# Optimization experiments

Measured on AMD Instinct MI355X. Metric: run time of the kernel, lower is better.

Reference implementation:

```python
import jax, jax.numpy as jnp
import numpy as np

N = 50000
E = 800000
IN_C, C1, C2 = 256, 128, 64
BN_EPS = 1e-5


def setup_inputs() -> dict:
    key = jax.random.key(0)
    ks = jax.random.split(key, 12)
    x = jax.random.normal(ks[0], (N, IN_C), dtype=jnp.float32)
    edge_index = jax.random.randint(ks[1], (2, E), 0, N, dtype=jnp.int32)
    edge_weight = jax.random.uniform(ks[2], (E,), dtype=jnp.float32)
    W1 = jax.random.normal(ks[3], (IN_C, C1), dtype=jnp.float32) * 0.05
    b1 = jnp.zeros((C1,), dtype=jnp.float32)
    W2 = jax.random.normal(ks[4], (C1, C2), dtype=jnp.float32) * 0.05
    b2 = jnp.zeros((C2,), dtype=jnp.float32)
    g1 = jnp.ones((C1,), dtype=jnp.float32)
    be1 = jnp.zeros((C1,), dtype=jnp.float32)
    g2 = jnp.ones((C2,), dtype=jnp.float32)
    be2 = jnp.zeros((C2,), dtype=jnp.float32)
    Ws = jax.random.normal(ks[5], (IN_C, C2), dtype=jnp.float32) * 0.05
    bs = jnp.zeros((C2,), dtype=jnp.float32)
    return dict(x=x, edge_index=edge_index, edge_weight=edge_weight,
                W1=W1, b1=b1, W2=W2, b2=b2, g1=g1, be1=be1, g2=g2, be2=be2,
                Ws=Ws, bs=bs)


def _gcn_conv(h_in, row, col, ew, W, b):
    # PyG GCNConv: transform then symmetric-normalized aggregation with self-loops
    n = h_in.shape[0]
    h = h_in @ W  # [N, C]
    loop = jnp.arange(n, dtype=row.dtype)
    row_f = jnp.concatenate([row, loop])
    col_f = jnp.concatenate([col, loop])
    ew_f = jnp.concatenate([ew, jnp.ones((n,), dtype=ew.dtype)])
    deg = jax.ops.segment_sum(ew_f, col_f, num_segments=n)  # degree at targets
    dinv = jnp.where(deg > 0, jax.lax.rsqrt(deg), 0.0)
    norm = dinv[row_f] * ew_f * dinv[col_f]  # [E+N]
    out = jax.ops.segment_sum(h[row_f] * norm[:, None], col_f, num_segments=n)
    return out + b


def _batchnorm(x, gamma, beta):
    mu = jnp.mean(x, axis=0)
    var = jnp.mean(jnp.square(x - mu), axis=0)  # biased, as torch BN forward
    return (x - mu) * jax.lax.rsqrt(var + BN_EPS) * gamma + beta


def reference(x, edge_index, edge_weight, W1, b1, W2, b2, g1, be1, g2, be2, Ws, bs):
    row, col = edge_index[0], edge_index[1]
    skip = x @ Ws + bs
    x1 = _gcn_conv(x, row, col, edge_weight, W1, b1)
    x1 = jax.nn.gelu(_batchnorm(x1, g1, be1), approximate=False)
    # dropout is identity in deterministic/eval reference
    x2 = _gcn_conv(x1, row, col, edge_weight, W2, b2)
    x2 = _batchnorm(x2, g2, be2) + skip
    return x2
```

## Files before the change

kernel.cpp:

```cpp
#include <hip/hip_runtime.h>
#include <math.h>

constexpr int NN = 50000;
constexpr int EE = 800000;
constexpr int INC = 256, CC1 = 128, CC2 = 64;

typedef short bf16x8 __attribute__((ext_vector_type(8)));
typedef float f32x4 __attribute__((ext_vector_type(4)));

__device__ __forceinline__ unsigned short f2bf(float f) {
    unsigned int u = __builtin_bit_cast(unsigned int, f);
    u = (u + 0x7FFFu + ((u >> 16) & 1u)) >> 16;
    return (unsigned short)u;
}
__device__ __forceinline__ float bflo(unsigned int w) {
    return __builtin_bit_cast(float, w << 16);
}
__device__ __forceinline__ float bfhi(unsigned int w) {
    return __builtin_bit_cast(float, w & 0xFFFF0000u);
}


__global__ void init_kernel(unsigned long long* __restrict__ packed,
                            float* __restrict__ stats, int* __restrict__ cursor, int n) {
    int i = blockIdx.x * 256 + threadIdx.x;
    if (i < 1024) stats[i] = 0.0f;
    if (i == 0) *cursor = 0;
    if (i < n) packed[i] = 0ULL;
}

__global__ void rank_kernel(const int* __restrict__ col, const float* __restrict__ ew,
                            unsigned long long* __restrict__ packed, int* __restrict__ rank,
                            int e_cnt) {
    int e = blockIdx.x * 256 + threadIdx.x;
    if (e < e_cnt) {
        int c = col[e];
        unsigned int fx = __float2uint_rn(ew[e] * 16777216.0f);
        unsigned long long old = atomicAdd(&packed[c], (1ULL << 32) | (unsigned long long)fx);
        rank[e] = (int)(old >> 32);
    }
}

__global__ void alloc_kernel(const unsigned long long* __restrict__ packed,
                             float* __restrict__ dinv, int* __restrict__ start,
                             int* __restrict__ count, int* __restrict__ cursor, int n) {
    int i = blockIdx.x * 256 + threadIdx.x;
    if (i < n) {
        unsigned long long p = packed[i];
        int cnt = (int)(p >> 32);
        float deg = 1.0f + (float)(unsigned int)(p & 0xFFFFFFFFu) * (1.0f / 16777216.0f);
        dinv[i] = rsqrtf(deg);
        count[i] = cnt;
        start[i] = atomicAdd(cursor, cnt);
    }
}

__global__ void fill_kernel(const int* __restrict__ row, const int* __restrict__ col,
                            const float* __restrict__ ew, const float* __restrict__ dinv,
                            const int* __restrict__ rank, const int* __restrict__ start,
                            int2* __restrict__ pairs, int e_cnt) {
    int e = blockIdx.x * 256 + threadIdx.x;
    if (e < e_cnt) {
        int r = row[e], c = col[e];
        float nv = dinv[r] * ew[e] * dinv[c];
        int pos = start[c] + rank[e];
        pairs[pos] = make_int2(r, __float_as_int(nv));
    }
}

template<int K, int N1, int N2, int AMODE>
__global__ void __launch_bounds__(256) mfma_gemm(const void* __restrict__ Av,
        const float* __restrict__ B1, const float* __restrict__ B2,
        unsigned short* __restrict__ C1, float* __restrict__ C2,
        const float* __restrict__ scA, const float* __restrict__ shA, int n_rows) {
    constexpr int NT = N1 + N2;
    constexpr int NG = 64;
    constexpr int KC = K / 8;
    constexpr int PITCH = K + 8;
    __shared__ unsigned short Blds[NG * PITCH];

    const int tid = threadIdx.x;
    const int wave = tid >> 6, lane = tid & 63;
    const int quad = lane >> 4, nIdx = lane & 15;
    const int row0 = blockIdx.x * 64 + wave * 16;
    const int arow = row0 + nIdx;
    const int arow_c = (arow < n_rows) ? arow : (n_rows - 1);

    bf16x8 afrag[K / 32];
    if (AMODE == 1) {
        const unsigned short* A = (const unsigned short*)Av;
        const unsigned short* ap = A + (long long)arow_c * K + quad * 8;
#pragma unroll
        for (int s = 0; s < K / 32; s++)
            afrag[s] = *(const bf16x8*)(ap + s * 32);
    } else {
        const float* A = (const float*)Av;
        const float* ap = A + (long long)arow_c * K + quad * 8;
#pragma unroll
        for (int s = 0; s < K / 32; s++) {
            float4 lo = *(const float4*)(ap + s * 32);
            float4 hi = *(const float4*)(ap + s * 32 + 4);
            float v[8] = {lo.x, lo.y, lo.z, lo.w, hi.x, hi.y, hi.z, hi.w};
            if (AMODE == 2) {
                int kb = s * 32 + quad * 8;
                float4 s0 = *(const float4*)(scA + kb);
                float4 s1 = *(const float4*)(scA + kb + 4);
                float4 t0 = *(const float4*)(shA + kb);
                float4 t1 = *(const float4*)(shA + kb + 4);
                float sc[8] = {s0.x, s0.y, s0.z, s0.w, s1.x, s1.y, s1.z, s1.w};
                float sh[8] = {t0.x, t0.y, t0.z, t0.w, t1.x, t1.y, t1.z, t1.w};
#pragma unroll
                for (int j = 0; j < 8; j++) {
                    float u = v[j] * sc[j] + sh[j];
                    v[j] = u * 0.5f * (1.0f + erff(u * 0.70710678f));
                }
            }
            bf16x8 f;
#pragma unroll
            for (int j = 0; j < 8; j++) f[j] = (short)f2bf(v[j]);
            afrag[s] = f;
        }
    }

    for (int g0 = 0; g0 < NT; g0 += NG) {
        if (g0) __syncthreads();
        {
            int n = tid & 63;
            int col = g0 + n;
            const float* Bp = B1; int Nw = N1; int bcol = col;
            if (N2 > 0 && col >= N1) { Bp = B2; Nw = N2; bcol = col - N1; }
            for (int kc = tid >> 6; kc < KC; kc += 4) {
                int k0 = kc * 8;
                bf16x8 v;
#pragma unroll
                for (int j = 0; j < 8; j++)
                    v[j] = (short)f2bf(Bp[(long long)(k0 + j) * Nw + bcol]);
                *(bf16x8*)(&Blds[n * PITCH + k0]) = v;
            }
        }
        __syncthreads();
#pragma unroll
        for (int t = 0; t < NG / 16; t++) {
            const unsigned short* bp = &Blds[(t * 16 + nIdx) * PITCH + quad * 8];
            f32x4 acc = {0.0f, 0.0f, 0.0f, 0.0f};
#pragma unroll
            for (int s = 0; s < K / 32; s++) {
                bf16x8 bf = *(const bf16x8*)(bp + s * 32);
                acc = __builtin_amdgcn_mfma_f32_16x16x32_bf16(afrag[s], bf, acc, 0, 0, 0);
            }
            int ocol = g0 + t * 16 + nIdx;
#pragma unroll
            for (int r = 0; r < 4; r++) {
                int orow = row0 + quad * 4 + r;
                if (orow < n_rows) {
                    if (N2 == 0 || ocol < N1)
                        C1[(long long)orow * N1 + ocol] = f2bf(acc[r]);
                    else
                        C2[(long long)orow * N2 + (ocol - N1)] = acc[r];
                }
            }
        }
    }
}

template<int C>
__global__ void gather_agg_bf16(const unsigned short* __restrict__ h, const float* __restrict__ dinv,
                                const float* __restrict__ b, const int2* __restrict__ pairs,
                                const int* __restrict__ start, const int* __restrict__ count,
                                float* __restrict__ out, int n) {
    constexpr int TPN = C / 8;
    int gid = blockIdx.x * 256 + threadIdx.x;
    int node = gid / TPN;
    int part = gid - node * TPN;
    if (node >= n) return;
    int c8 = part * 8;
    float d = dinv[node];
    float d2 = d * d;
    uint4 hv = *(const uint4*)(h + (long long)node * C + c8);
    float a0 = bflo(hv.x) * d2 + b[c8 + 0];
    float a1 = bfhi(hv.x) * d2 + b[c8 + 1];
    float a2 = bflo(hv.y) * d2 + b[c8 + 2];
    float a3 = bfhi(hv.y) * d2 + b[c8 + 3];
    float a4 = bflo(hv.z) * d2 + b[c8 + 4];
    float a5 = bfhi(hv.z) * d2 + b[c8 + 5];
    float a6 = bflo(hv.w) * d2 + b[c8 + 6];
    float a7 = bfhi(hv.w) * d2 + b[c8 + 7];
    const int2* pp = pairs + start[node];
    int m = count[node];
    int j = 0;
    for (; j + 4 <= m; j += 4) {
        int2 p0 = pp[j + 0], p1 = pp[j + 1], p2 = pp[j + 2], p3 = pp[j + 3];
        uint4 v0 = *(const uint4*)(h + (long long)p0.x * C + c8);
        uint4 v1 = *(const uint4*)(h + (long long)p1.x * C + c8);
        uint4 v2 = *(const uint4*)(h + (long long)p2.x * C + c8);
        uint4 v3 = *(const uint4*)(h + (long long)p3.x * C + c8);
        float w0 = __int_as_float(p0.y), w1 = __int_as_float(p1.y);
        float w2 = __int_as_float(p2.y), w3 = __int_as_float(p3.y);
        a0 += bflo(v0.x) * w0; a1 += bfhi(v0.x) * w0;
        a2 += bflo(v0.y) * w0; a3 += bfhi(v0.y) * w0;
        a4 += bflo(v0.z) * w0; a5 += bfhi(v0.z) * w0;
        a6 += bflo(v0.w) * w0; a7 += bfhi(v0.w) * w0;
        a0 += bflo(v1.x) * w1; a1 += bfhi(v1.x) * w1;
        a2 += bflo(v1.y) * w1; a3 += bfhi(v1.y) * w1;
        a4 += bflo(v1.z) * w1; a5 += bfhi(v1.z) * w1;
        a6 += bflo(v1.w) * w1; a7 += bfhi(v1.w) * w1;
        a0 += bflo(v2.x) * w2; a1 += bfhi(v2.x) * w2;
        a2 += bflo(v2.y) * w2; a3 += bfhi(v2.y) * w2;
        a4 += bflo(v2.z) * w2; a5 += bfhi(v2.z) * w2;
        a6 += bflo(v2.w) * w2; a7 += bfhi(v2.w) * w2;
        a0 += bflo(v3.x) * w3; a1 += bfhi(v3.x) * w3;
        a2 += bflo(v3.y) * w3; a3 += bfhi(v3.y) * w3;
        a4 += bflo(v3.z) * w3; a5 += bfhi(v3.z) * w3;
        a6 += bflo(v3.w) * w3; a7 += bfhi(v3.w) * w3;
    }
    for (; j < m; j++) {
        int2 p = pp[j];
        float w = __int_as_float(p.y);
        uint4 v = *(const uint4*)(h + (long long)p.x * C + c8);
        a0 += bflo(v.x) * w; a1 += bfhi(v.x) * w;
        a2 += bflo(v.y) * w; a3 += bfhi(v.y) * w;
        a4 += bflo(v.z) * w; a5 += bfhi(v.z) * w;
        a6 += bflo(v.w) * w; a7 += bfhi(v.w) * w;
    }
    float4 o0 = {a0, a1, a2, a3}, o1 = {a4, a5, a6, a7};
    *(float4*)(out + (long long)node * C + c8) = o0;
    *(float4*)(out + (long long)node * C + c8 + 4) = o1;
}


template<int C>
__global__ void bnstats_kernel(const float* __restrict__ x, float* __restrict__ sum,
                               float* __restrict__ sumsq, int n) {
    constexpr int RG = 256 / C;
    constexpr int ROWS = 128;
    const int c = threadIdx.x % C;
    const int rg = threadIdx.x / C;
    const int base = blockIdx.x * ROWS;
    float s = 0.0f, ss = 0.0f;
    for (int r = rg; r < ROWS; r += RG) {
        int nn = base + r;
        if (nn < n) {
            float v = x[(long long)nn * C + c];
            s += v; ss += v * v;
        }
    }
    __shared__ float ls[256], lss[256];
    ls[threadIdx.x] = s; lss[threadIdx.x] = ss;
    __syncthreads();
    if (rg == 0) {
#pragma unroll
        for (int g = 1; g < RG; g++) { s += ls[g * C + c]; ss += lss[g * C + c]; }
        atomicAdd(&sum[c], s);
        atomicAdd(&sumsq[c], ss);
    }
}

__global__ void bnparams_kernel(const float* __restrict__ sum, const float* __restrict__ sumsq,
                                const float* __restrict__ gamma, const float* __restrict__ beta,
                                const float* __restrict__ extra_bias,
                                float* __restrict__ scale, float* __restrict__ shift,
                                int n, int c_cnt) {
    int c = threadIdx.x;
    if (c < c_cnt) {
        float inv_n = 1.0f / (float)n;
        float mu = sum[c] * inv_n;
        float var = sumsq[c] * inv_n - mu * mu;
        if (var < 0.0f) var = 0.0f;
        float sc = gamma[c] * rsqrtf(var + 1e-5f);
        float sh = beta[c] - mu * sc;
        if (extra_bias) sh += extra_bias[c];
        scale[c] = sc; shift[c] = sh;
    }
}

template<int C>
__global__ void final_kernel(const float* __restrict__ x, const float* __restrict__ scale,
                             const float* __restrict__ shift, const float* __restrict__ skip,
                             float* __restrict__ out, int total) {
    int i = blockIdx.x * 256 + threadIdx.x;
    if (i >= total) return;
    int c = i % C;
    out[i] = x[i] * scale[c] + shift[c] + skip[i];
}


extern "C" void kernel_launch(void* const* d_in, const int* in_sizes, int n_in,
                              void* d_out, int out_size, void* d_ws, size_t ws_size,
                              hipStream_t stream) {
    const float* x   = (const float*)d_in[0];
    const int*   ei  = (const int*)d_in[1];
    const float* ew  = (const float*)d_in[2];
    const float* W1  = (const float*)d_in[3];
    const float* b1  = (const float*)d_in[4];
    const float* W2  = (const float*)d_in[5];
    const float* b2  = (const float*)d_in[6];
    const float* g1  = (const float*)d_in[7];
    const float* be1 = (const float*)d_in[8];
    const float* g2  = (const float*)d_in[9];
    const float* be2 = (const float*)d_in[10];
    const float* Ws  = (const float*)d_in[11];
    const float* bs  = (const float*)d_in[12];
    float* out = (float*)d_out;

    const int* row = ei;
    const int* col = ei + EE;

    float* w = (float*)d_ws;
    float* dinv    = w;
    float* agg1    = dinv + NN;
    float* agg2    = agg1 + (long long)NN * CC1;
    float* skip    = agg2 + (long long)NN * CC2;
    float* stats   = skip + (long long)NN * CC2;
    unsigned long long* packed = (unsigned long long*)(stats + 1024);
    int*   rank    = (int*)(packed + NN);
    int*   startp  = rank + EE;
    int*   countp  = startp + NN;
    int*   cursor  = countp + NN;
    int2*  pairs   = (int2*)(cursor + 4);
    unsigned short* h1b = (unsigned short*)(pairs + EE);
    unsigned short* h2b = h1b + (long long)NN * CC1;

    float* sum1   = stats;
    float* sumsq1 = stats + 128;
    float* sum2   = stats + 256;
    float* sumsq2 = stats + 320;
    float* scale1 = stats + 384;
    float* shift1 = stats + 512;
    float* scale2 = stats + 640;
    float* shift2 = stats + 704;

    const int nb_N = (NN + 255) / 256;
    const int nb_E = (EE + 255) / 256;
    const int nb_G = (NN + 63) / 64;

    init_kernel<<<nb_N, 256, 0, stream>>>(packed, stats, cursor, NN);
    rank_kernel<<<nb_E, 256, 0, stream>>>(col, ew, packed, rank, EE);
    alloc_kernel<<<nb_N, 256, 0, stream>>>(packed, dinv, startp, countp, cursor, NN);
    fill_kernel<<<nb_E, 256, 0, stream>>>(row, col, ew, dinv, rank, startp, pairs, EE);

    mfma_gemm<INC, CC1, CC2, 0><<<nb_G, 256, 0, stream>>>(x, W1, Ws, h1b, skip,
                                                          nullptr, nullptr, NN);
    gather_agg_bf16<CC1><<<(NN * (CC1 / 8) + 255) / 256, 256, 0, stream>>>(
        h1b, dinv, b1, pairs, startp, countp, agg1, NN);

    bnstats_kernel<CC1><<<(NN + 127) / 128, 256, 0, stream>>>(agg1, sum1, sumsq1, NN);
    bnparams_kernel<<<1, 128, 0, stream>>>(sum1, sumsq1, g1, be1, nullptr, scale1, shift1, NN, CC1);

    mfma_gemm<CC1, CC2, 0, 2><<<nb_G, 256, 0, stream>>>(agg1, W2, W2, h2b, nullptr,
                                                        scale1, shift1, NN);
    gather_agg_bf16<CC2><<<(NN * (CC2 / 8) + 255) / 256, 256, 0, stream>>>(
        h2b, dinv, b2, pairs, startp, countp, agg2, NN);

    bnstats_kernel<CC2><<<(NN + 127) / 128, 256, 0, stream>>>(agg2, sum2, sumsq2, NN);
    bnparams_kernel<<<1, 64, 0, stream>>>(sum2, sumsq2, g2, be2, bs, scale2, shift2, NN, CC2);
    final_kernel<CC2><<<(NN * CC2 + 255) / 256, 256, 0, stream>>>(agg2, scale2, shift2, skip, out, NN * CC2);

    (void)in_sizes; (void)n_in; (void)out_size; (void)ws_size;
}
```

Before: 334.5 us.

## Fuse rank counting into first GEMM, store intermediates in bf16, fold BN params

Merges the edge-rank atomic pass into the first GEMM launch as extra blocks, and replaces the init kernel with a memset. Aggregation outputs and the skip path are stored as bf16 instead of fp32, which roughly halves traffic for BN stats, GEMM2 and the final kernel. The bnparams kernels are removed by computing scale and shift inside GEMM2 and the final kernel, and the gather loop is unrolled to 8 edges. In exchange, aggregates and the skip term are rounded to bf16 before BN, which adds precision error.

After: 317.6 us. 5.1% less time.

```diff
diff --git a/kernel.cpp b/kernel.cpp
--- a/kernel.cpp
+++ b/kernel.cpp
@@ -13,33 +13,104 @@
     u = (u + 0x7FFFu + ((u >> 16) & 1u)) >> 16;
     return (unsigned short)u;
 }
+__device__ __forceinline__ float bf2f(unsigned short u) {
+    return __builtin_bit_cast(float, (unsigned int)u << 16);
+}
 __device__ __forceinline__ float bflo(unsigned int w) {
     return __builtin_bit_cast(float, w << 16);
 }
 __device__ __forceinline__ float bfhi(unsigned int w) {
     return __builtin_bit_cast(float, w & 0xFFFF0000u);
 }
-
-
-__global__ void init_kernel(unsigned long long* __restrict__ packed,
-                            float* __restrict__ stats, int* __restrict__ cursor, int n) {
-    int i = blockIdx.x * 256 + threadIdx.x;
-    if (i < 1024) stats[i] = 0.0f;
-    if (i == 0) *cursor = 0;
-    if (i < n) packed[i] = 0ULL;
-}
-
-__global__ void rank_kernel(const int* __restrict__ col, const float* __restrict__ ew,
-                            unsigned long long* __restrict__ packed, int* __restrict__ rank,
-                            int e_cnt) {
-    int e = blockIdx.x * 256 + threadIdx.x;
-    if (e < e_cnt) {
-        int c = col[e];
-        unsigned int fx = __float2uint_rn(ew[e] * 16777216.0f);
-        unsigned long long old = atomicAdd(&packed[c], (1ULL << 32) | (unsigned long long)fx);
-        rank[e] = (int)(old >> 32);
-    }
-}
+__device__ __forceinline__ unsigned int packbf2(float lo, float hi) {
+    return (unsigned int)f2bf(lo) | ((unsigned int)f2bf(hi) << 16);
+}
+
+__global__ void __launch_bounds__(256) gemm1_rank_kernel(
+        const float* __restrict__ A, const float* __restrict__ B1, const float* __restrict__ B2,
+        unsigned short* __restrict__ C1, unsigned short* __restrict__ C2,
+        const int* __restrict__ col, const float* __restrict__ ew,
+        unsigned long long* __restrict__ packed, int* __restrict__ rank, int gemm_blocks) {
+    constexpr int K = INC, N1 = CC1, N2 = CC2, NT = N1 + N2;
+    constexpr int NG = 64, KC = K / 8, PITCH = K + 8;
+    __shared__ unsigned short Blds[NG * PITCH];
+
+    if ((int)blockIdx.x >= gemm_blocks) {
+        int e = (blockIdx.x - gemm_blocks) * 256 + threadIdx.x;
+        if (e < EE) {
+            int c = col[e];
+            unsigned int fx = __float2uint_rn(ew[e] * 16777216.0f);
+            unsigned long long old =
+                atomicAdd(&packed[c], (1ULL << 32) | (unsigned long long)fx);
+            rank[e] = (int)(old >> 32);
+        }
+        return;
+    }
+
+    const int tid = threadIdx.x;
+    const int wave = tid >> 6, lane = tid & 63;
+    const int quad = lane >> 4, nIdx = lane & 15;
+    const int row0 = blockIdx.x * 64 + wave * 16;
+    const int arow = row0 + nIdx;
+    const int arow_c = (arow < NN) ? arow : (NN - 1);
+
+    bf16x8 afrag[K / 32];
+    {
+        const float* ap = A + (long long)arow_c * K + quad * 8;
+#pragma unroll
+        for (int s = 0; s < K / 32; s++) {
+            float4 lo = *(const float4*)(ap + s * 32);
+            float4 hi = *(const float4*)(ap + s * 32 + 4);
+            bf16x8 f;
+            f[0] = (short)f2bf(lo.x); f[1] = (short)f2bf(lo.y);
+            f[2] = (short)f2bf(lo.z); f[3] = (short)f2bf(lo.w);
+            f[4] = (short)f2bf(hi.x); f[5] = (short)f2bf(hi.y);
+            f[6] = (short)f2bf(hi.z); f[7] = (short)f2bf(hi.w);
+            afrag[s] = f;
+        }
+    }
+
+    for (int g0 = 0; g0 < NT; g0 += NG) {
+        if (g0) __syncthreads();
+        {
+            int n = tid & 63;
+            int gcol = g0 + n;
+            const float* Bp = B1; int Nw = N1; int bcol = gcol;
+            if (gcol >= N1) { Bp = B2; Nw = N2; bcol = gcol - N1; }
+            for (int kc = tid >> 6; kc < KC; kc += 4) {
+                int k0 = kc * 8;
+                bf16x8 v;
+#pragma unroll
+                for (int j = 0; j < 8; j++)
+                    v[j] = (short)f2bf(Bp[(long long)(k0 + j) * Nw + bcol]);
+                *(bf16x8*)(&Blds[n * PITCH + k0]) = v;
+            }
+        }
+        __syncthreads();
+#pragma unroll
+        for (int t = 0; t < NG / 16; t++) {
+            const unsigned short* bp = &Blds[(t * 16 + nIdx) * PITCH + quad * 8];
+            f32x4 acc = {0.0f, 0.0f, 0.0f, 0.0f};
+#pragma unroll
+            for (int s = 0; s < K / 32; s++) {
+                bf16x8 bf = *(const bf16x8*)(bp + s * 32);
+                acc = __builtin_amdgcn_mfma_f32_16x16x32_bf16(afrag[s], bf, acc, 0, 0, 0);
+            }
+            int ocol = g0 + t * 16 + nIdx;
+#pragma unroll
+            for (int r = 0; r < 4; r++) {
+                int orow = row0 + quad * 4 + r;
+                if (orow < NN) {
+                    if (ocol < N1)
+                        C1[(long long)orow * N1 + ocol] = f2bf(acc[r]);
+                    else
+                        C2[(long long)orow * N2 + (ocol - N1)] = f2bf(acc[r]);
+                }
+            }
+        }
+    }
+}
+
 
 __global__ void alloc_kernel(const unsigned long long* __restrict__ packed,
                              float* __restrict__ dinv, int* __restrict__ start,
@@ -68,18 +139,37 @@
     }
 }
 
-template<int K, int N1, int N2, int AMODE>
-__global__ void __launch_bounds__(256) mfma_gemm(const void* __restrict__ Av,
-        const float* __restrict__ B1, const float* __restrict__ B2,
-        unsigned short* __restrict__ C1, float* __restrict__ C2,
-        const float* __restrict__ scA, const float* __restrict__ shA, int n_rows) {
-    constexpr int NT = N1 + N2;
-    constexpr int NG = 64;
-    constexpr int KC = K / 8;
-    constexpr int PITCH = K + 8;
-    __shared__ unsigned short Blds[NG * PITCH];
+__global__ void __launch_bounds__(256) gemm2_kernel(
+        const unsigned short* __restrict__ A, const float* __restrict__ B,
+        unsigned short* __restrict__ C,
+        const float* __restrict__ sum, const float* __restrict__ sumsq,
+        const float* __restrict__ gamma, const float* __restrict__ beta, int n_rows) {
+    constexpr int K = CC1, N = CC2;
+    constexpr int KC = K / 8, PITCH = K + 8;
+    __shared__ unsigned short Blds[N * PITCH];
+    __shared__ float scL[K], shL[K];
 
     const int tid = threadIdx.x;
+    if (tid < K) {
+        float inv_n = 1.0f / (float)n_rows;
+        float mu = sum[tid] * inv_n;
+        float var = fmaxf(sumsq[tid] * inv_n - mu * mu, 0.0f);
+        float sc = gamma[tid] * rsqrtf(var + 1e-5f);
+        scL[tid] = sc; shL[tid] = beta[tid] - mu * sc;
+    }
+    {
+        int n = tid & 63;
+        for (int kc = tid >> 6; kc < KC; kc += 4) {
+            int k0 = kc * 8;
+            bf16x8 v;
+#pragma unroll
+            for (int j = 0; j < 8; j++)
+                v[j] = (short)f2bf(B[(long long)(k0 + j) * N + n]);
+            *(bf16x8*)(&Blds[n * PITCH + k0]) = v;
+        }
+    }
+    __syncthreads();
+
     const int wave = tid >> 6, lane = tid & 63;
     const int quad = lane >> 4, nIdx = lane & 15;
     const int row0 = blockIdx.x * 64 + wave * 16;
@@ -87,87 +177,46 @@
     const int arow_c = (arow < n_rows) ? arow : (n_rows - 1);
 
     bf16x8 afrag[K / 32];
-    if (AMODE == 1) {
-        const unsigned short* A = (const unsigned short*)Av;
+    {
         const unsigned short* ap = A + (long long)arow_c * K + quad * 8;
 #pragma unroll
-        for (int s = 0; s < K / 32; s++)
-            afrag[s] = *(const bf16x8*)(ap + s * 32);
-    } else {
-        const float* A = (const float*)Av;
-        const float* ap = A + (long long)arow_c * K + quad * 8;
-#pragma unroll
         for (int s = 0; s < K / 32; s++) {
-            float4 lo = *(const float4*)(ap + s * 32);
-            float4 hi = *(const float4*)(ap + s * 32 + 4);
-            float v[8] = {lo.x, lo.y, lo.z, lo.w, hi.x, hi.y, hi.z, hi.w};
-            if (AMODE == 2) {
-                int kb = s * 32 + quad * 8;
-                float4 s0 = *(const float4*)(scA + kb);
-                float4 s1 = *(const float4*)(scA + kb + 4);
-                float4 t0 = *(const float4*)(shA + kb);
-                float4 t1 = *(const float4*)(shA + kb + 4);
-                float sc[8] = {s0.x, s0.y, s0.z, s0.w, s1.x, s1.y, s1.z, s1.w};
-                float sh[8] = {t0.x, t0.y, t0.z, t0.w, t1.x, t1.y, t1.z, t1.w};
-#pragma unroll
-                for (int j = 0; j < 8; j++) {
-                    float u = v[j] * sc[j] + sh[j];
-                    v[j] = u * 0.5f * (1.0f + erff(u * 0.70710678f));
-                }
+            bf16x8 raw = *(const bf16x8*)(ap + s * 32);
+            int kb = s * 32 + quad * 8;
+            bf16x8 f;
+#pragma unroll
+            for (int j = 0; j < 8; j++) {
+                float u = bf2f((unsigned short)raw[j]) * scL[kb + j] + shL[kb + j];
+                float v = u * 0.5f * (1.0f + erff(u * 0.70710678f));
+                f[j] = (short)f2bf(v);
             }
-            bf16x8 f;
-#pragma unroll
-            for (int j = 0; j < 8; j++) f[j] = (short)f2bf(v[j]);
             afrag[s] = f;
         }
     }
-
-    for (int g0 = 0; g0 < NT; g0 += NG) {
-        if (g0) __syncthreads();
-        {
-            int n = tid & 63;
-            int col = g0 + n;
-            const float* Bp = B1; int Nw = N1; int bcol = col;
-            if (N2 > 0 && col >= N1) { Bp = B2; Nw = N2; bcol = col - N1; }
-            for (int kc = tid >> 6; kc < KC; kc += 4) {
-                int k0 = kc * 8;
-                bf16x8 v;
-#pragma unroll
-                for (int j = 0; j < 8; j++)
-                    v[j] = (short)f2bf(Bp[(long long)(k0 + j) * Nw + bcol]);
-                *(bf16x8*)(&Blds[n * PITCH + k0]) = v;
-            }
-        }
-        __syncthreads();
-#pragma unroll
-        for (int t = 0; t < NG / 16; t++) {
-            const unsigned short* bp = &Blds[(t * 16 + nIdx) * PITCH + quad * 8];
-            f32x4 acc = {0.0f, 0.0f, 0.0f, 0.0f};
-#pragma unroll
-            for (int s = 0; s < K / 32; s++) {
-                bf16x8 bf = *(const bf16x8*)(bp + s * 32);
-                acc = __builtin_amdgcn_mfma_f32_16x16x32_bf16(afrag[s], bf, acc, 0, 0, 0);
-            }
-            int ocol = g0 + t * 16 + nIdx;
-#pragma unroll
-            for (int r = 0; r < 4; r++) {
-                int orow = row0 + quad * 4 + r;
-                if (orow < n_rows) {
-                    if (N2 == 0 || ocol < N1)
-                        C1[(long long)orow * N1 + ocol] = f2bf(acc[r]);
-                    else
-                        C2[(long long)orow * N2 + (ocol - N1)] = acc[r];
-                }
-            }
+#pragma unroll
+    for (int t = 0; t < N / 16; t++) {
+        const unsigned short* bp = &Blds[(t * 16 + nIdx) * PITCH + quad * 8];
+        f32x4 acc = {0.0f, 0.0f, 0.0f, 0.0f};
+#pragma unroll
+        for (int s = 0; s < K / 32; s++) {
+            bf16x8 bf = *(const bf16x8*)(bp + s * 32);
+            acc = __builtin_amdgcn_mfma_f32_16x16x32_bf16(afrag[s], bf, acc, 0, 0, 0);
+        }
+        int ocol = t * 16 + nIdx;
+#pragma unroll
+        for (int r = 0; r < 4; r++) {
+            int orow = row0 + quad * 4 + r;
+            if (orow < n_rows)
+                C[(long long)orow * N + ocol] = f2bf(acc[r]);
         }
     }
 }
 
 template<int C>
-__global__ void gather_agg_bf16(const unsigned short* __restrict__ h, const float* __restrict__ dinv,
-                                const float* __restrict__ b, const int2* __restrict__ pairs,
-                                const int* __restrict__ start, const int* __restrict__ count,
-                                float* __restrict__ out, int n) {
+__global__ void gather_agg(const unsigned short* __restrict__ h, const float* __restrict__ dinv,
+                           const float* __restrict__ b, const int2* __restrict__ pairs,
+                           const int* __restrict__ start, const int* __restrict__ count,
+                           unsigned short* __restrict__ outb, int n) {
     constexpr int TPN = C / 8;
     int gid = blockIdx.x * 256 + threadIdx.x;
     int node = gid / TPN;
@@ -188,30 +237,22 @@
     const int2* pp = pairs + start[node];
     int m = count[node];
     int j = 0;
-    for (; j + 4 <= m; j += 4) {
-        int2 p0 = pp[j + 0], p1 = pp[j + 1], p2 = pp[j + 2], p3 = pp[j + 3];
-        uint4 v0 = *(const uint4*)(h + (long long)p0.x * C + c8);
-        uint4 v1 = *(const uint4*)(h + (long long)p1.x * C + c8);
-        uint4 v2 = *(const uint4*)(h + (long long)p2.x * C + c8);
-        uint4 v3 = *(const uint4*)(h + (long long)p3.x * C + c8);
-        float w0 = __int_as_float(p0.y), w1 = __int_as_float(p1.y);
-        float w2 = __int_as_float(p2.y), w3 = __int_as_float(p3.y);
-        a0 += bflo(v0.x) * w0; a1 += bfhi(v0.x) * w0;
-        a2 += bflo(v0.y) * w0; a3 += bfhi(v0.y) * w0;
-        a4 += bflo(v0.z) * w0; a5 += bfhi(v0.z) * w0;
-        a6 += bflo(v0.w) * w0; a7 += bfhi(v0.w) * w0;
-        a0 += bflo(v1.x) * w1; a1 += bfhi(v1.x) * w1;
-        a2 += bflo(v1.y) * w1; a3 += bfhi(v1.y) * w1;
-        a4 += bflo(v1.z) * w1; a5 += bfhi(v1.z) * w1;
-        a6 += bflo(v1.w) * w1; a7 += bfhi(v1.w) * w1;
-        a0 += bflo(v2.x) * w2; a1 += bfhi(v2.x) * w2;
-        a2 += bflo(v2.y) * w2; a3 += bfhi(v2.y) * w2;
-        a4 += bflo(v2.z) * w2; a5 += bfhi(v2.z) * w2;
-        a6 += bflo(v2.w) * w2; a7 += bfhi(v2.w) * w2;
-        a0 += bflo(v3.x) * w3; a1 += bfhi(v3.x) * w3;
-        a2 += bflo(v3.y) * w3; a3 += bfhi(v3.y) * w3;
-        a4 += bflo(v3.z) * w3; a5 += bfhi(v3.z) * w3;
-        a6 += bflo(v3.w) * w3; a7 += bfhi(v3.w) * w3;
+    for (; j + 8 <= m; j += 8) {
+        int2 p[8];
+#pragma unroll
+        for (int i = 0; i < 8; i++) p[i] = pp[j + i];
+        uint4 v[8];
+#pragma unroll
+        for (int i = 0; i < 8; i++)
+            v[i] = *(const uint4*)(h + (long long)p[i].x * C + c8);
+#pragma unroll
+        for (int i = 0; i < 8; i++) {
+            float w = __int_as_float(p[i].y);
+            a0 += bflo(v[i].x) * w; a1 += bfhi(v[i].x) * w;
+            a2 += bflo(v[i].y) * w; a3 += bfhi(v[i].y) * w;
+            a4 += bflo(v[i].z) * w; a5 += bfhi(v[i].z) * w;
+            a6 += bflo(v[i].w) * w; a7 += bfhi(v[i].w) * w;
+        }
     }
     for (; j < m; j++) {
         int2 p = pp[j];
@@ -222,65 +263,70 @@
         a4 += bflo(v.z) * w; a5 += bfhi(v.z) * w;
         a6 += bflo(v.w) * w; a7 += bfhi(v.w) * w;
     }
-    float4 o0 = {a0, a1, a2, a3}, o1 = {a4, a5, a6, a7};
-    *(float4*)(out + (long long)node * C + c8) = o0;
-    *(float4*)(out + (long long)node * C + c8 + 4) = o1;
-}
-
+    uint4 o;
+    o.x = packbf2(a0, a1); o.y = packbf2(a2, a3);
+    o.z = packbf2(a4, a5); o.w = packbf2(a6, a7);
+    *(uint4*)(outb + (long long)node * C + c8) = o;
+}
 
 template<int C>
-__global__ void bnstats_kernel(const float* __restrict__ x, float* __restrict__ sum,
-                               float* __restrict__ sumsq, int n) {
-    constexpr int RG = 256 / C;
-    constexpr int ROWS = 128;
-    const int c = threadIdx.x % C;
-    const int rg = threadIdx.x / C;
+__global__ void bnstats_bf16(const unsigned short* __restrict__ x, float* __restrict__ sum,
+                             float* __restrict__ sumsq, int n) {
+    constexpr int PR = C / 2;
+    constexpr int RG = 256 / PR;
+    constexpr int ROWS = 256;
+    const int cp = threadIdx.x % PR;
+    const int rg = threadIdx.x / PR;
     const int base = blockIdx.x * ROWS;
-    float s = 0.0f, ss = 0.0f;
+    const unsigned int* xu = (const unsigned int*)x;
+    float s0 = 0, ss0 = 0, s1 = 0, ss1 = 0;
     for (int r = rg; r < ROWS; r += RG) {
         int nn = base + r;
         if (nn < n) {
-            float v = x[(long long)nn * C + c];
-            s += v; ss += v * v;
-        }
-    }
-    __shared__ float ls[256], lss[256];
-    ls[threadIdx.x] = s; lss[threadIdx.x] = ss;
+            unsigned int v = xu[(long long)nn * PR + cp];
+            float lo = bflo(v), hi = bfhi(v);
+            s0 += lo; ss0 += lo * lo; s1 += hi; ss1 += hi * hi;
+        }
+    }
+    __shared__ float red[4][256];
+    red[0][threadIdx.x] = s0; red[1][threadIdx.x] = ss0;
+    red[2][threadIdx.x] = s1; red[3][threadIdx.x] = ss1;
     __syncthreads();
     if (rg == 0) {
 #pragma unroll
-        for (int g = 1; g < RG; g++) { s += ls[g * C + c]; ss += lss[g * C + c]; }
-        atomicAdd(&sum[c], s);
-        atomicAdd(&sumsq[c], ss);
-    }
-}
-
-__global__ void bnparams_kernel(const float* __restrict__ sum, const float* __restrict__ sumsq,
-                                const float* __restrict__ gamma, const float* __restrict__ beta,
-                                const float* __restrict__ extra_bias,
-                                float* __restrict__ scale, float* __restrict__ shift,
-                                int n, int c_cnt) {
-    int c = threadIdx.x;
-    if (c < c_cnt) {
+        for (int g = 1; g < RG; g++) {
+            s0 += red[0][g * PR + cp]; ss0 += red[1][g * PR + cp];
+            s1 += red[2][g * PR + cp]; ss1 += red[3][g * PR + cp];
+        }
+        atomicAdd(&sum[2 * cp], s0);     atomicAdd(&sumsq[2 * cp], ss0);
+        atomicAdd(&sum[2 * cp + 1], s1); atomicAdd(&sumsq[2 * cp + 1], ss1);
+    }
+}
+
+__global__ void final_kernel(const unsigned short* __restrict__ agg2b,
+                             const unsigned short* __restrict__ skipb,
+                             const float* __restrict__ sum, const float* __restrict__ sumsq,
+                             const float* __restrict__ gamma, const float* __restrict__ beta,
+                             const float* __restrict__ bs, float* __restrict__ out, int n) {
+    __shared__ float sc[CC2], sh[CC2];
+    if (threadIdx.x < CC2) {
         float inv_n = 1.0f / (float)n;
-        float mu = sum[c] * inv_n;
-        float var = sumsq[c] * inv_n - mu * mu;
-        if (var < 0.0f) var = 0.0f;
-        float sc = gamma[c] * rsqrtf(var + 1e-5f);
-        float sh = beta[c] - mu * sc;
-        if (extra_bias) sh += extra_bias[c];
-        scale[c] = sc; shift[c] = sh;
-    }
-}
-
-template<int C>
-__global__ void final_kernel(const float* __restrict__ x, const float* __restrict__ scale,
-                             const float* __restrict__ shift, const float* __restrict__ skip,
-                             float* __restrict__ out, int total) {
-    int i = blockIdx.x * 256 + threadIdx.x;
-    if (i >= total) return;
-    int c = i % C;
-    out[i] = x[i] * scale[c] + shift[c] + skip[i];
+        float mu = sum[threadIdx.x] * inv_n;
+        float var = fmaxf(sumsq[threadIdx.x] * inv_n - mu * mu, 0.0f);
+        float s = gamma[threadIdx.x] * rsqrtf(var + 1e-5f);
+        sc[threadIdx.x] = s;
+        sh[threadIdx.x] = beta[threadIdx.x] - mu * s + bs[threadIdx.x];
+    }
+    __syncthreads();
+    int i2 = blockIdx.x * 256 + threadIdx.x;
+    if (i2 >= n * (CC2 / 2)) return;
+    unsigned int av = ((const unsigned int*)agg2b)[i2];
+    unsigned int sv = ((const unsigned int*)skipb)[i2];
+    int c2 = (i2 % (CC2 / 2)) * 2;
+    float2 o;
+    o.x = bflo(av) * sc[c2] + sh[c2] + bflo(sv);
+    o.y = bfhi(av) * sc[c2 + 1] + sh[c2 + 1] + bfhi(sv);
+    *(float2*)(out + 2 * (long long)i2) = o;
 }
 
 
@@ -305,55 +351,49 @@
     const int* row = ei;
     const int* col = ei + EE;
 
-    float* w = (float*)d_ws;
-    float* dinv    = w;
-    float* agg1    = dinv + NN;
-    float* agg2    = agg1 + (long long)NN * CC1;
-    float* skip    = agg2 + (long long)NN * CC2;
-    float* stats   = skip + (long long)NN * CC2;
-    unsigned long long* packed = (unsigned long long*)(stats + 1024);
-    int*   rank    = (int*)(packed + NN);
-    int*   startp  = rank + EE;
-    int*   countp  = startp + NN;
-    int*   cursor  = countp + NN;
-    int2*  pairs   = (int2*)(cursor + 4);
-    unsigned short* h1b = (unsigned short*)(pairs + EE);
-    unsigned short* h2b = h1b + (long long)NN * CC1;
-
+    char* wp = (char*)d_ws;
+    float* stats = (float*)wp;
     float* sum1   = stats;
     float* sumsq1 = stats + 128;
     float* sum2   = stats + 256;
     float* sumsq2 = stats + 320;
-    float* scale1 = stats + 384;
-    float* shift1 = stats + 512;
-    float* scale2 = stats + 640;
-    float* shift2 = stats + 704;
+    int*   cursor = (int*)(wp + 4096);
+    unsigned long long* packed = (unsigned long long*)(wp + 4112);
+    char* p2 = wp + 4112 + (size_t)NN * 8;
+    int*   rank   = (int*)p2;             p2 += (size_t)EE * 4;
+    int*   startp = (int*)p2;             p2 += (size_t)NN * 4;
+    int*   countp = (int*)p2;             p2 += (size_t)NN * 4;
+    float* dinv   = (float*)p2;           p2 += (size_t)NN * 4;
+    int2*  pairs  = (int2*)p2;            p2 += (size_t)EE * 8;
+    unsigned short* h1b   = (unsigned short*)p2; p2 += (size_t)NN * CC1 * 2;
+    unsigned short* h2b   = (unsigned short*)p2; p2 += (size_t)NN * CC2 * 2;
+    unsigned short* agg1b = (unsigned short*)p2; p2 += (size_t)NN * CC1 * 2;
+    unsigned short* agg2b = (unsigned short*)p2; p2 += (size_t)NN * CC2 * 2;
+    unsigned short* skipb = (unsigned short*)p2; p2 += (size_t)NN * CC2 * 2;
 
     const int nb_N = (NN + 255) / 256;
     const int nb_E = (EE + 255) / 256;
     const int nb_G = (NN + 63) / 64;
 
-    init_kernel<<<nb_N, 256, 0, stream>>>(packed, stats, cursor, NN);
-    rank_kernel<<<nb_E, 256, 0, stream>>>(col, ew, packed, rank, EE);
+    hipMemsetAsync(wp, 0, 4112 + (size_t)NN * 8, stream);
+
+    gemm1_rank_kernel<<<nb_G + nb_E, 256, 0, stream>>>(
+        x, W1, Ws, h1b, skipb, col, ew, packed, rank, nb_G);
+
     alloc_kernel<<<nb_N, 256, 0, stream>>>(packed, dinv, startp, countp, cursor, NN);
     fill_kernel<<<nb_E, 256, 0, stream>>>(row, col, ew, dinv, rank, startp, pairs, EE);
 
-    mfma_gemm<INC, CC1, CC2, 0><<<nb_G, 256, 0, stream>>>(x, W1, Ws, h1b, skip,
-                                                          nullptr, nullptr, NN);
-    gather_agg_bf16<CC1><<<(NN * (CC1 / 8) + 255) / 256, 256, 0, stream>>>(
-        h1b, dinv, b1, pairs, startp, countp, agg1, NN);
-
-    bnstats_kernel<CC1><<<(NN + 127) / 128, 256, 0, stream>>>(agg1, sum1, sumsq1, NN);
-    bnparams_kernel<<<1, 128, 0, stream>>>(sum1, sumsq1, g1, be1, nullptr, scale1, shift1, NN, CC1);
-
-    mfma_gemm<CC1, CC2, 0, 2><<<nb_G, 256, 0, stream>>>(agg1, W2, W2, h2b, nullptr,
-                                                        scale1, shift1, NN);
-    gather_agg_bf16<CC2><<<(NN * (CC2 / 8) + 255) / 256, 256, 0, stream>>>(
-        h2b, dinv, b2, pairs, startp, countp, agg2, NN);
-
-    bnstats_kernel<CC2><<<(NN + 127) / 128, 256, 0, stream>>>(agg2, sum2, sumsq2, NN);
-    bnparams_kernel<<<1, 64, 0, stream>>>(sum2, sumsq2, g2, be2, bs, scale2, shift2, NN, CC2);
-    final_kernel<CC2><<<(NN * CC2 + 255) / 256, 256, 0, stream>>>(agg2, scale2, shift2, skip, out, NN * CC2);
+    gather_agg<CC1><<<(NN * (CC1 / 8) + 255) / 256, 256, 0, stream>>>(
+        h1b, dinv, b1, pairs, startp, countp, agg1b, NN);
+    bnstats_bf16<CC1><<<(NN + 255) / 256, 256, 0, stream>>>(agg1b, sum1, sumsq1, NN);
+
+    gemm2_kernel<<<nb_G, 256, 0, stream>>>(agg1b, W2, h2b, sum1, sumsq1, g1, be1, NN);
+    gather_agg<CC2><<<(NN * (CC2 / 8) + 255) / 256, 256, 0, stream>>>(
+        h2b, dinv, b2, pairs, startp, countp, agg2b, NN);
+    bnstats_bf16<CC2><<<(NN + 255) / 256, 256, 0, stream>>>(agg2b, sum2, sumsq2, NN);
+
+    final_kernel<<<(NN * (CC2 / 2) + 255) / 256, 256, 0, stream>>>(
+        agg2b, skipb, sum2, sumsq2, g2, be2, bs, out, NN);
 
     (void)in_sizes; (void)n_in; (void)out_size; (void)ws_size;
 }
```
